# Kernel tuning notes

Measured on AMD Instinct MI355X. Metric: run time of the kernel, lower is better.

## Reference

```python
import jax, jax.numpy as jnp
import numpy as np

HIDDEN = 256
MAX_LENGTH = 256
NUM_LAYERS = 4
VOCAB = 50257


def setup_inputs() -> dict:
    key = jax.random.key(0)
    ks = jax.random.split(key, 16)
    s = 0.05
    return {
        "token": jax.random.randint(ks[0], (1,), 0, VOCAB, dtype=jnp.int64 if jax.config.jax_enable_x64 else jnp.int32),
        "hidden": jax.random.normal(ks[1], (NUM_LAYERS, 1, HIDDEN), dtype=jnp.float32),
        "encoder_outputs": jax.random.normal(ks[2], (MAX_LENGTH, HIDDEN), dtype=jnp.float32),
        "emb": jax.random.normal(ks[3], (VOCAB, HIDDEN), dtype=jnp.float32) * s,
        "attn_w": jax.random.normal(ks[4], (MAX_LENGTH, 2 * HIDDEN), dtype=jnp.float32) * s,
        "attn_b": jax.random.normal(ks[5], (MAX_LENGTH,), dtype=jnp.float32) * s,
        "comb_w": jax.random.normal(ks[6], (HIDDEN, 2 * HIDDEN), dtype=jnp.float32) * s,
        "comb_b": jax.random.normal(ks[7], (HIDDEN,), dtype=jnp.float32) * s,
        "gru_wih": jax.random.normal(ks[8], (NUM_LAYERS, 3 * HIDDEN, HIDDEN), dtype=jnp.float32) * s,
        "gru_whh": jax.random.normal(ks[9], (NUM_LAYERS, 3 * HIDDEN, HIDDEN), dtype=jnp.float32) * s,
        "gru_bih": jax.random.normal(ks[10], (NUM_LAYERS, 3 * HIDDEN), dtype=jnp.float32) * s,
        "gru_bhh": jax.random.normal(ks[11], (NUM_LAYERS, 3 * HIDDEN), dtype=jnp.float32) * s,
        "out_w": jax.random.normal(ks[12], (VOCAB, HIDDEN), dtype=jnp.float32) * s,
        "out_b": jax.random.normal(ks[13], (VOCAB,), dtype=jnp.float32) * s,
    }


def _gru_cell(x, h, wih, whh, bih, bhh):
    # PyTorch GRU cell: gates ordered [r, z, n]
    gi = x @ wih.T + bih  # [1, 3H]
    gh = h @ whh.T + bhh  # [1, 3H]
    i_r, i_z, i_n = jnp.split(gi, 3, axis=1)
    h_r, h_z, h_n = jnp.split(gh, 3, axis=1)
    r = jax.nn.sigmoid(i_r + h_r)
    z = jax.nn.sigmoid(i_z + h_z)
    n = jnp.tanh(i_n + r * h_n)
    return (1.0 - z) * n + z * h


def reference(token, hidden, encoder_outputs, emb, attn_w, attn_b, comb_w, comb_b,
              gru_wih, gru_whh, gru_bih, gru_bhh, out_w, out_b):
    # embedding lookup (dropout is identity in eval)  -> [1, H]
    embedded = emb[token]
    # Bahdanau-style attention weights over MAX_LENGTH positions
    attn_in = jnp.concatenate([embedded, hidden[0]], axis=1)  # [1, 2H]
    attn_weights = jax.nn.softmax(attn_in @ attn_w.T + attn_b, axis=1)  # [1, L]
    attn_applied = attn_weights @ encoder_outputs  # [1, H]
    comb_in = jnp.concatenate([embedded, attn_applied], axis=1)  # [1, 2H]
    x = jax.nn.relu(comb_in @ comb_w.T + comb_b)  # [1, H]
    # 4-layer GRU, single timestep
    new_h = []
    for l in range(NUM_LAYERS):
        h_l = _gru_cell(x, hidden[l], gru_wih[l], gru_whh[l], gru_bih[l], gru_bhh[l])
        new_h.append(h_l)
        x = h_l
    hidden_new = jnp.stack(new_h, axis=0)  # [4, 1, H]
    logp = jax.nn.log_softmax(x @ out_w.T + out_b, axis=1)  # [1, V]
    return (logp, hidden_new, attn_weights)
```

## Files before the change

### kernel.cpp

```cpp
#include <hip/hip_runtime.h>
#include <hip/hip_bf16.h>

#define H 256
#define L2H 512
#define NLAYERS 4
#define VOCAB 50257

#define OUT_LOGP 0
#define OUT_HID  50257
#define OUT_ATTN 51281

#define WS_SCORE 0
#define WS_BARS  256
#define WS_APP   512
#define WS_XA    768
#define WS_XB    1024
#define WS_PM    768
#define WS_PS    1024
#define WS_X4    1280
#define WS_X4B   1536
#define WS_X4C   1792
#define WS_GO    2048
#define WS_FLAG  2304

#define L_SCORE 0
#define L_APP   1
#define L_X0    2
#define L_LOG0  8

#define NCHAIN 8
#define NBLK 256

typedef unsigned short u16;
typedef unsigned long long u64;

__device__ __forceinline__ float bf2f(u16 u) {
    return __uint_as_float(((unsigned int)u) << 16);
}

__device__ __forceinline__ u16 f2bf(float f) {
    unsigned int x = __float_as_uint(f);
    unsigned int r = x + 0x7fff + ((x >> 16) & 1);
    return (u16)(r >> 16);
}

template<bool BF16>
__device__ __forceinline__ float ld1(const void* p, size_t i) {
    if (BF16) return bf2f(((const u16*)p)[i]);
    else      return ((const float*)p)[i];
}

template<bool BF16>
__device__ __forceinline__ void ld8(const void* p, size_t i, float* f) {
    if (BF16) {
        uint4 u = *(const uint4*)((const u16*)p + i);
        f[0] = bf2f(u.x & 0xffff); f[1] = bf2f(u.x >> 16);
        f[2] = bf2f(u.y & 0xffff); f[3] = bf2f(u.y >> 16);
        f[4] = bf2f(u.z & 0xffff); f[5] = bf2f(u.z >> 16);
        f[6] = bf2f(u.w & 0xffff); f[7] = bf2f(u.w >> 16);
    } else {
        const float4* q = (const float4*)((const float*)p + i);
        float4 a = q[0], b = q[1];
        f[0] = a.x; f[1] = a.y; f[2] = a.z; f[3] = a.w;
        f[4] = b.x; f[5] = b.y; f[6] = b.z; f[7] = b.w;
    }
}

template<bool BF16>
__device__ __forceinline__ void st(void* p, size_t i, float v) {
    if (BF16) ((u16*)p)[i] = f2bf(v);
    else      ((float*)p)[i] = v;
}

__device__ __forceinline__ float ldc(const float* p) {
    return __hip_atomic_load(const_cast<float*>(p), __ATOMIC_RELAXED, __HIP_MEMORY_SCOPE_AGENT);
}
__device__ __forceinline__ void stc(float* p, float v) {
    __hip_atomic_store(p, v, __ATOMIC_RELAXED, __HIP_MEMORY_SCOPE_AGENT);
}
__device__ __forceinline__ u64 ldcu(const u64* p) {
    return __hip_atomic_load(const_cast<u64*>(p), __ATOMIC_RELAXED, __HIP_MEMORY_SCOPE_AGENT);
}
__device__ __forceinline__ void stcu(u64* p, u64 v) {
    __hip_atomic_store(p, v, __ATOMIC_RELAXED, __HIP_MEMORY_SCOPE_AGENT);
}

__device__ __forceinline__ void arrive_line(unsigned* bars, int idx) {
    __syncthreads();
    if (threadIdx.x == 0)
        __hip_atomic_fetch_add(&bars[idx * 16], 1u, __ATOMIC_RELAXED, __HIP_MEMORY_SCOPE_AGENT);
}
template<int SLP>
__device__ __forceinline__ void wait_line(unsigned* bars, int idx, unsigned exp) {
    if (threadIdx.x == 0) {
        while (__hip_atomic_load(&bars[idx * 16], __ATOMIC_RELAXED, __HIP_MEMORY_SCOPE_AGENT) < exp)
            __builtin_amdgcn_s_sleep(SLP);
    }
    __syncthreads();
}

template<int SLP>
__device__ __forceinline__ u64 poll_go(const u64* p, unsigned need) {
    u64 u = ldcu(p);
    while ((unsigned)(u & 0xffffffffull) < need) {
        __builtin_amdgcn_s_sleep(SLP);
        u = ldcu(p);
    }
    return u;
}

__device__ __forceinline__ float dot8_u4bf(uint4 u, const float* xf) {
    return bf2f(u.x & 0xffff)*xf[0] + bf2f(u.x >> 16)*xf[1]
         + bf2f(u.y & 0xffff)*xf[2] + bf2f(u.y >> 16)*xf[3]
         + bf2f(u.z & 0xffff)*xf[4] + bf2f(u.z >> 16)*xf[5]
         + bf2f(u.w & 0xffff)*xf[6] + bf2f(u.w >> 16)*xf[7];
}

__global__ __launch_bounds__(256) void k_init(const void* emb, float* ws) {
    int tid = threadIdx.x;
    __hip_atomic_store((unsigned*)(ws + WS_BARS) + tid, 0u, __ATOMIC_RELAXED, __HIP_MEMORY_SCOPE_AGENT);
    __hip_atomic_store((unsigned*)(ws + WS_GO) + tid, 0u, __ATOMIC_RELAXED, __HIP_MEMORY_SCOPE_AGENT);
    __hip_atomic_store((unsigned*)(ws + WS_APP) + tid, 0u, __ATOMIC_RELAXED, __HIP_MEMORY_SCOPE_AGENT);
    if (tid < 64) {
        float b = fabsf(bf2f(((const u16*)emb)[tid]));
        #pragma unroll
        for (int off = 32; off; off >>= 1) b = fmaxf(b, __shfl_xor(b, off));
        if (tid == 0) ws[WS_FLAG] = (b < 1.0f) ? 1.0f : 0.0f;
    }
}

template<bool BF16>
__device__ __forceinline__ void logits_stream(
    const void* __restrict__ out_w, const void* __restrict__ out_b,
    const float* xf, int grp, int l32, float* vs, float& m, float& s)
{
    #pragma unroll
    for (int it = 0; it < 3; ++it) {
        const int rb = it * 16384 + grp;
        float wf[8][8], bb[8];
        #pragma unroll
        for (int k = 0; k < 8; ++k) {
            ld8<BF16>(out_w, (size_t)(rb + (k << 11)) * H + l32 * 8, wf[k]);
            bb[k] = ld1<BF16>(out_b, rb + (k << 11));
        }
        #pragma unroll
        for (int k = 0; k < 8; ++k) {
            float v = wf[k][0]*xf[0] + wf[k][1]*xf[1] + wf[k][2]*xf[2] + wf[k][3]*xf[3]
                    + wf[k][4]*xf[4] + wf[k][5]*xf[5] + wf[k][6]*xf[6] + wf[k][7]*xf[7];
            #pragma unroll
            for (int off = 16; off; off >>= 1) v += __shfl_xor(v, off);
            v += bb[k];
            vs[it * 8 + k] = v;
            float mn = fmaxf(m, v);
            s = s * __expf(m - mn) + __expf(v - mn);
            m = mn;
        }
    }
    vs[24] = 0.f;
    if (grp < VOCAB - 49152) {
        int r = 49152 + grp;
        float wf[8]; ld8<BF16>(out_w, (size_t)r * H + l32 * 8, wf);
        float v = wf[0]*xf[0] + wf[1]*xf[1] + wf[2]*xf[2] + wf[3]*xf[3]
                + wf[4]*xf[4] + wf[5]*xf[5] + wf[6]*xf[6] + wf[7]*xf[7];
        #pragma unroll
        for (int off = 16; off; off >>= 1) v += __shfl_xor(v, off);
        v += ld1<BF16>(out_b, r);
        vs[24] = v;
        float mn = fmaxf(m, v);
        s = s * __expf(m - mn) + __expf(v - mn);
        m = mn;
    }
}

template<bool BF16>
__device__ __forceinline__ void pipeline(
    const int* __restrict__ tok, const void* __restrict__ emb,
    const void* __restrict__ hidden,
    const void* __restrict__ attn_w, const void* __restrict__ attn_b,
    const void* __restrict__ enc,
    const void* __restrict__ comb_w, const void* __restrict__ comb_b,
    const void* __restrict__ gwih, const void* __restrict__ gwhh,
    const void* __restrict__ gbih, const void* __restrict__ gbhh,
    const void* __restrict__ out_w, const void* __restrict__ out_b,
    float* __restrict__ ws, void* __restrict__ out)
{
    unsigned* bars = (unsigned*)(ws + WS_BARS);
    const int tid  = threadIdx.x;
    const int lane = tid & 63;
    const int wid  = tid >> 6;
    const int bx   = blockIdx.x;
    const size_t es = BF16 ? 2 : 4;

    const int grp = (bx << 3) | (tid >> 5);
    const int l32 = tid & 31;

    __shared__ float lds[256];
    __shared__ float wsm[256];
    __shared__ float xsh[256];
    __shared__ float hsh[256];
    __shared__ float gd[192];
    __shared__ float cshare;

    float vs[25];
    float m = -1e30f, s = 0.f;

    if (bx < NCHAIN) {
        const int rbase = bx * 32;
        const int j8 = lane * 8;
        const int tk = tok[0];

        {
            float wfa[8][8];
            #pragma unroll
            for (int k = 0; k < 8; ++k)
                ld8<BF16>(attn_w, (size_t)(rbase + wid * 8 + k) * L2H + j8, wfa[k]);
            float xin[8];
            if (lane < 32) ld8<BF16>(emb, (size_t)tk * H + j8, xin);
            else           ld8<BF16>(hidden, (size_t)(j8 - H), xin);
            #pragma unroll
            for (int k = 0; k < 8; ++k) {
                int r = rbase + wid * 8 + k;
                float v = 0.f;
                #pragma unroll
                for (int q = 0; q < 8; ++q) v += xin[q] * wfa[k][q];
                #pragma unroll
                for (int off = 32; off; off >>= 1) v += __shfl_xor(v, off);
                if (lane == 0) stc(ws + WS_SCORE + r, v + ld1<BF16>(attn_b, r));
            }
        }
        arrive_line(bars, L_SCORE);

        {
            float ev[32];
            #pragma unroll
            for (int k = 0; k < 32; ++k)
                ev[k] = ld1<BF16>(enc, (size_t)(rbase + k) * H + tid);
            wait_line<1>(bars, L_SCORE, NCHAIN);
            float sc = ldc(ws + WS_SCORE + tid);
            lds[tid] = sc; __syncthreads();
            for (int off = 128; off; off >>= 1) {
                if (tid < off) lds[tid] = fmaxf(lds[tid], lds[tid + off]);
                __syncthreads();
            }
            float M = lds[0]; __syncthreads();
            float e = __expf(sc - M);
            lds[tid] = e; __syncthreads();
            for (int off = 128; off; off >>= 1) {
                if (tid < off) lds[tid] += lds[tid + off];
                __syncthreads();
            }
            float w = e / lds[0];
            wsm[tid] = w; __syncthreads();
            if (bx == 0) st<BF16>(out, OUT_ATTN + tid, w);
            float acc = 0.f;
            #pragma unroll
            for (int k = 0; k < 32; ++k) acc += wsm[rbase + k] * ev[k];
            atomicAdd(&ws[WS_APP + tid], acc);
        }
        arrive_line(bars, L_APP);

        {
            float wfa[8][8];
            #pragma unroll
            for (int k = 0; k < 8; ++k)
                ld8<BF16>(comb_w, (size_t)(rbase + wid * 8 + k) * L2H + j8, wfa[k]);
            float xin[8];
            if (lane < 32) ld8<BF16>(emb, (size_t)tk * H + j8, xin);
            wait_line<1>(bars, L_APP, NCHAIN);
            xsh[tid] = ldc(ws + WS_APP + tid);
            __syncthreads();
            if (lane >= 32) {
                #pragma unroll
                for (int q = 0; q < 8; ++q) xin[q] = xsh[j8 - H + q];
            }
            #pragma unroll
            for (int k = 0; k < 8; ++k) {
                int r = rbase + wid * 8 + k;
                float v = 0.f;
                #pragma unroll
                for (int q = 0; q < 8; ++q) v += xin[q] * wfa[k][q];
                #pragma unroll
                for (int off = 32; off; off >>= 1) v += __shfl_xor(v, off);
                if (lane == 0) stc(ws + WS_XA + r, fmaxf(v + ld1<BF16>(comb_b, r), 0.f));
            }
        }
        arrive_line(bars, L_X0);

        #pragma unroll 1
        for (int l = 0; l < NLAYERS; ++l) {
            const float* xin_p = ws + ((l & 1) ? WS_XB : WS_XA);
            const char* wih = (const char*)gwih + (size_t)l * 3 * H * H * es;
            const char* whh = (const char*)gwhh + (size_t)l * 3 * H * H * es;
            const char* bih = (const char*)gbih + (size_t)l * 3 * H * es;
            const char* bhh = (const char*)gbhh + (size_t)l * 3 * H * es;
            const char* hprev = (const char*)hidden + (size_t)l * H * es;
            char*       hout  = (char*)out + (size_t)(OUT_HID + l * H) * es;

            wait_line<1>(bars, L_X0 + l, NCHAIN);
            xsh[tid] = ldc(xin_p + tid);
            hsh[tid] = ld1<BF16>(hprev, tid);
            __syncthreads();

            if (tid < 192) {
                int mat = tid / 96;
                int rem = tid % 96;
                int g   = rem / 32;
                int j   = rem % 32;
                const void* W = mat ? (const void*)whh : (const void*)wih;
                const float* xv = mat ? hsh : xsh;
                size_t rowoff = (size_t)(g * H + rbase + j) * H;
                float acc = 0.f;
                #pragma unroll 16
                for (int c = 0; c < H; c += 8) {
                    float wf[8]; ld8<BF16>(W, rowoff + c, wf);
                    acc += wf[0]*xv[c]   + wf[1]*xv[c+1] + wf[2]*xv[c+2] + wf[3]*xv[c+3]
                         + wf[4]*xv[c+4] + wf[5]*xv[c+5] + wf[6]*xv[c+6] + wf[7]*xv[c+7];
                }
                gd[tid] = acc;
            }
            __syncthreads();
            if (tid < 32) {
                int i = rbase + tid;
                float r = 1.f / (1.f + __expf(-(gd[tid]      + ld1<BF16>(bih, i)
                                              + gd[96 + tid] + ld1<BF16>(bhh, i))));
                float z = 1.f / (1.f + __expf(-(gd[32 + tid]  + ld1<BF16>(bih, H + i)
                                              + gd[128 + tid] + ld1<BF16>(bhh, H + i))));
                float n = tanhf(gd[64 + tid] + ld1<BF16>(bih, 2 * H + i)
                              + r * (gd[160 + tid] + ld1<BF16>(bhh, 2 * H + i)));
                float hn = (1.f - z) * n + z * hsh[i];
                if (l < 3) stc(ws + ((l & 1) ? WS_XA : WS_XB) + i, hn);
                else { stc(ws + WS_X4 + i, hn); stc(ws + WS_X4B + i, hn); stc(ws + WS_X4C + i, hn); }
                st<BF16>(hout, i, hn);
            }
            arrive_line(bars, L_X0 + l + 1);
        }

        wait_line<1>(bars, L_X0 + 4, NCHAIN);
        if (bx == 0 && tid < 16)
            stcu((u64*)(ws + WS_GO + 16 * tid), 1ull);

        xsh[tid] = ldc(ws + WS_X4 + (bx % 3) * 256 + tid);
        __syncthreads();
        float xf[8];
        #pragma unroll
        for (int q = 0; q < 8; ++q) xf[q] = xsh[l32 * 8 + q];
        logits_stream<BF16>(out_w, out_b, xf, grp, l32, vs, m, s);
    } else {
        if constexpr (BF16) {
            uint4 pw[25]; float pb[25];
            #pragma unroll
            for (int it = 0; it < 3; ++it)
                #pragma unroll
                for (int k = 0; k < 8; ++k) {
                    int r = it * 16384 + (k << 11) + grp;
                    pw[it * 8 + k] = *(const uint4*)((const u16*)out_w + (size_t)r * H + l32 * 8);
                    pb[it * 8 + k] = ld1<true>(out_b, r);
                }
            if (grp < VOCAB - 49152) {
                int r = 49152 + grp;
                pw[24] = *(const uint4*)((const u16*)out_w + (size_t)r * H + l32 * 8);
                pb[24] = ld1<true>(out_b, r);
            } else { pw[24] = make_uint4(0, 0, 0, 0); pb[24] = 0.f; }

            if (tid == 0) (void)poll_go<2>((const u64*)(ws + WS_GO + 16 * (bx & 15)), 1u);
            __syncthreads();
            xsh[tid] = ldc(ws + WS_X4 + (bx % 3) * 256 + tid);
            __syncthreads();
            float xf[8];
            #pragma unroll
            for (int q = 0; q < 8; ++q) xf[q] = xsh[l32 * 8 + q];

            #pragma unroll
            for (int idx = 0; idx < 24; ++idx) {
                float v = dot8_u4bf(pw[idx], xf);
                #pragma unroll
                for (int off = 16; off; off >>= 1) v += __shfl_xor(v, off);
                v += pb[idx];
                vs[idx] = v;
                float mn = fmaxf(m, v);
                s = s * __expf(m - mn) + __expf(v - mn);
                m = mn;
            }
            vs[24] = 0.f;
            if (grp < VOCAB - 49152) {
                float v = dot8_u4bf(pw[24], xf);
                #pragma unroll
                for (int off = 16; off; off >>= 1) v += __shfl_xor(v, off);
                v += pb[24];
                vs[24] = v;
                float mn = fmaxf(m, v);
                s = s * __expf(m - mn) + __expf(v - mn);
                m = mn;
            }
        } else {
            if (tid == 0) (void)poll_go<2>((const u64*)(ws + WS_GO + 16 * (bx & 15)), 1u);
            __syncthreads();
            xsh[tid] = ldc(ws + WS_X4 + (bx % 3) * 256 + tid);
            __syncthreads();
            float xf[8];
            #pragma unroll
            for (int q = 0; q < 8; ++q) xf[q] = xsh[l32 * 8 + q];
            logits_stream<false>(out_w, out_b, xf, grp, l32, vs, m, s);
        }
    }

    {
        float mo = __shfl_xor(m, 32), so = __shfl_xor(s, 32);
        float M = fmaxf(m, mo);
        s = s * __expf(m - M) + so * __expf(mo - M);
        m = M;
    }
    if (lane == 0) { lds[wid] = m; lds[4 + wid] = s; }
    __syncthreads();
    if (tid == 0) {
        float M01 = fmaxf(lds[0], lds[1]);
        float S01 = lds[4] * __expf(lds[0] - M01) + lds[5] * __expf(lds[1] - M01);
        float M23 = fmaxf(lds[2], lds[3]);
        float S23 = lds[6] * __expf(lds[2] - M23) + lds[7] * __expf(lds[3] - M23);
        float Mx = fmaxf(M01, M23);
        float S  = S01 * __expf(M01 - Mx) + S23 * __expf(M23 - Mx);
        stc(ws + WS_PM + bx, Mx);
        stc(ws + WS_PS + bx, S);
    }
    arrive_line(bars, L_LOG0 + (bx & 7));

    float c;
    if (bx == 0) {
        if (tid < 8) {
            while (__hip_atomic_load(&bars[(L_LOG0 + tid) * 16],
                                     __ATOMIC_RELAXED, __HIP_MEMORY_SCOPE_AGENT) < 32u)
                __builtin_amdgcn_s_sleep(1);
        }
        __syncthreads();
        float mm = ldc(ws + WS_PM + tid);
        float ss = ldc(ws + WS_PS + tid);
        #pragma unroll
        for (int off = 32; off; off >>= 1) {
            float mo = __shfl_xor(mm, off), so = __shfl_xor(ss, off);
            float M = fmaxf(mm, mo);
            ss = ss * __expf(mm - M) + so * __expf(mo - M);
            mm = M;
        }
        if (lane == 0) { lds[wid] = mm; lds[4 + wid] = ss; }
        __syncthreads();
        if (tid == 0) {
            float M01 = fmaxf(lds[0], lds[1]);
            float S01 = lds[4] * __expf(lds[0] - M01) + lds[5] * __expf(lds[1] - M01);
            float M23 = fmaxf(lds[2], lds[3]);
            float S23 = lds[6] * __expf(lds[2] - M23) + lds[7] * __expf(lds[3] - M23);
            float Mx = fmaxf(M01, M23);
            float S  = S01 * __expf(M01 - Mx) + S23 * __expf(M23 - Mx);
            cshare = Mx + __logf(S);
        }
        __syncthreads();
        c = cshare;
        if (tid < 16)
            stcu((u64*)(ws + WS_GO + 16 * tid),
                 ((u64)__float_as_uint(c) << 32) | 2ull);
    } else {
        if (tid == 0) {
            u64 u = poll_go<2>((const u64*)(ws + WS_GO + 16 * (bx & 15)), 2u);
            cshare = __uint_as_float((unsigned)(u >> 32));
        }
        __syncthreads();
        c = cshare;
    }

    if (l32 == 0) {
        #pragma unroll
        for (int it = 0; it < 3; ++it)
            #pragma unroll
            for (int k = 0; k < 8; ++k)
                st<BF16>(out, OUT_LOGP + it * 16384 + (k << 11) + grp, vs[it * 8 + k] - c);
        if (grp < VOCAB - 49152)
            st<BF16>(out, OUT_LOGP + 49152 + grp, vs[24] - c);
    }
}

__global__ __launch_bounds__(256, 1) void k_all(
    const int* __restrict__ tok, const void* __restrict__ emb,
    const void* __restrict__ hidden,
    const void* __restrict__ attn_w, const void* __restrict__ attn_b,
    const void* __restrict__ enc,
    const void* __restrict__ comb_w, const void* __restrict__ comb_b,
    const void* __restrict__ gwih, const void* __restrict__ gwhh,
    const void* __restrict__ gbih, const void* __restrict__ gbhh,
    const void* __restrict__ out_w, const void* __restrict__ out_b,
    float* __restrict__ ws, void* __restrict__ out)
{
    if (ws[WS_FLAG] > 0.5f)
        pipeline<true >(tok, emb, hidden, attn_w, attn_b, enc, comb_w, comb_b,
                        gwih, gwhh, gbih, gbhh, out_w, out_b, ws, out);
    else
        pipeline<false>(tok, emb, hidden, attn_w, attn_b, enc, comb_w, comb_b,
                        gwih, gwhh, gbih, gbhh, out_w, out_b, ws, out);
}

extern "C" void kernel_launch(void* const* d_in, const int* in_sizes, int n_in,
                              void* d_out, int out_size, void* d_ws, size_t ws_size,
                              hipStream_t stream) {
    const int* tok = (const int*)d_in[0];
    float* ws = (float*)d_ws;

    k_init<<<dim3(1), dim3(256), 0, stream>>>(d_in[3], ws);
    k_all<<<dim3(NBLK), dim3(256), 0, stream>>>(
        tok, d_in[3], d_in[1], d_in[4], d_in[5], d_in[2], d_in[6], d_in[7],
        d_in[8], d_in[9], d_in[10], d_in[11], d_in[12], d_in[13],
        ws, d_out);
}
```

Baseline: 200.5 us.

## Spread decoder chain across 64 blocks with one row per wavefront

```diff
diff --git a/kernel.cpp b/kernel.cpp
--- a/kernel.cpp
+++ b/kernel.cpp
@@ -18,18 +18,16 @@
 #define WS_PM    768
 #define WS_PS    1024
 #define WS_X4    1280
-#define WS_X4B   1536
-#define WS_X4C   1792
 #define WS_GO    2048
 #define WS_FLAG  2304
 
-#define L_SCORE 0
-#define L_APP   1
-#define L_X0    2
-#define L_LOG0  8
-
-#define NCHAIN 8
-#define NBLK 256
+#define PH_SCORE 0
+#define PH_APP   1
+#define PH_X0    2
+#define PH_LOG   7
+
+#define NCHAIN 64
+#define NBLK   256
 
 typedef unsigned short u16;
 typedef unsigned long long u64;
@@ -48,6 +46,16 @@
 __device__ __forceinline__ float ld1(const void* p, size_t i) {
     if (BF16) return bf2f(((const u16*)p)[i]);
     else      return ((const float*)p)[i];
+}
+
+template<bool BF16>
+__device__ __forceinline__ float4 ld4(const void* p, size_t i) {
+    if (BF16) {
+        ushort4 w = *(const ushort4*)((const u16*)p + i);
+        return make_float4(bf2f(w.x), bf2f(w.y), bf2f(w.z), bf2f(w.w));
+    } else {
+        return *(const float4*)((const float*)p + i);
+    }
 }
 
 template<bool BF16>
@@ -85,15 +93,26 @@
     __hip_atomic_store(p, v, __ATOMIC_RELAXED, __HIP_MEMORY_SCOPE_AGENT);
 }
 
-__device__ __forceinline__ void arrive_line(unsigned* bars, int idx) {
+__device__ __forceinline__ void stage256(float* sh, const float* src, int tid) {
+    if (tid < 128) {
+        u64 u = ldcu((const u64*)src + tid);
+        sh[2 * tid]     = __uint_as_float((unsigned)(u & 0xffffffffull));
+        sh[2 * tid + 1] = __uint_as_float((unsigned)(u >> 32));
+    }
+    __syncthreads();
+}
+
+__device__ __forceinline__ void arrive_ph(unsigned* bars, int bx, int ph) {
     __syncthreads();
     if (threadIdx.x == 0)
-        __hip_atomic_fetch_add(&bars[idx * 16], 1u, __ATOMIC_RELAXED, __HIP_MEMORY_SCOPE_AGENT);
+        __hip_atomic_fetch_add(&bars[(bx & 15) * 16 + ph], 1u,
+                               __ATOMIC_RELAXED, __HIP_MEMORY_SCOPE_AGENT);
 }
 template<int SLP>
-__device__ __forceinline__ void wait_line(unsigned* bars, int idx, unsigned exp) {
-    if (threadIdx.x == 0) {
-        while (__hip_atomic_load(&bars[idx * 16], __ATOMIC_RELAXED, __HIP_MEMORY_SCOPE_AGENT) < exp)
+__device__ __forceinline__ void wait_ph(unsigned* bars, int ph, unsigned exp) {
+    if (threadIdx.x < 16) {
+        while (__hip_atomic_load(&bars[threadIdx.x * 16 + ph],
+                                 __ATOMIC_RELAXED, __HIP_MEMORY_SCOPE_AGENT) < exp)
             __builtin_amdgcn_s_sleep(SLP);
     }
     __syncthreads();
@@ -195,49 +214,42 @@
     const int l32 = tid & 31;
 
     __shared__ float lds[256];
+    __shared__ float xsh[256];
     __shared__ float wsm[256];
-    __shared__ float xsh[256];
-    __shared__ float hsh[256];
-    __shared__ float gd[192];
     __shared__ float cshare;
 
     float vs[25];
     float m = -1e30f, s = 0.f;
 
     if (bx < NCHAIN) {
-        const int rbase = bx * 32;
+        const int wv = (bx << 2) | wid;
         const int j8 = lane * 8;
         const int tk = tok[0];
 
         {
-            float wfa[8][8];
-            #pragma unroll
-            for (int k = 0; k < 8; ++k)
-                ld8<BF16>(attn_w, (size_t)(rbase + wid * 8 + k) * L2H + j8, wfa[k]);
+            float wf[8]; ld8<BF16>(attn_w, (size_t)wv * L2H + j8, wf);
             float xin[8];
             if (lane < 32) ld8<BF16>(emb, (size_t)tk * H + j8, xin);
             else           ld8<BF16>(hidden, (size_t)(j8 - H), xin);
-            #pragma unroll
-            for (int k = 0; k < 8; ++k) {
-                int r = rbase + wid * 8 + k;
-                float v = 0.f;
-                #pragma unroll
-                for (int q = 0; q < 8; ++q) v += xin[q] * wfa[k][q];
-                #pragma unroll
-                for (int off = 32; off; off >>= 1) v += __shfl_xor(v, off);
-                if (lane == 0) stc(ws + WS_SCORE + r, v + ld1<BF16>(attn_b, r));
-            }
-        }
-        arrive_line(bars, L_SCORE);
-
-        {
-            float ev[32];
-            #pragma unroll
-            for (int k = 0; k < 32; ++k)
-                ev[k] = ld1<BF16>(enc, (size_t)(rbase + k) * H + tid);
-            wait_line<1>(bars, L_SCORE, NCHAIN);
-            float sc = ldc(ws + WS_SCORE + tid);
-            lds[tid] = sc; __syncthreads();
+            float v = 0.f;
+            #pragma unroll
+            for (int q = 0; q < 8; ++q) v += xin[q] * wf[q];
+            #pragma unroll
+            for (int off = 32; off; off >>= 1) v += __shfl_xor(v, off);
+            if (lane == 0) stc(ws + WS_SCORE + wv, v + ld1<BF16>(attn_b, wv));
+        }
+        arrive_ph(bars, bx, PH_SCORE);
+
+        if (bx < 16) {
+            const int l0 = bx * 16;
+            float ev[16];
+            #pragma unroll
+            for (int k = 0; k < 16; ++k)
+                ev[k] = ld1<BF16>(enc, (size_t)(l0 + k) * H + tid);
+            wait_ph<1>(bars, PH_SCORE, 4);
+            stage256(lds, ws + WS_SCORE, tid);
+            float sc = lds[tid];
+            __syncthreads();
             for (int off = 128; off; off >>= 1) {
                 if (tid < off) lds[tid] = fmaxf(lds[tid], lds[tid + off]);
                 __syncthreads();
@@ -254,93 +266,93 @@
             if (bx == 0) st<BF16>(out, OUT_ATTN + tid, w);
             float acc = 0.f;
             #pragma unroll
-            for (int k = 0; k < 32; ++k) acc += wsm[rbase + k] * ev[k];
+            for (int k = 0; k < 16; ++k) acc += wsm[l0 + k] * ev[k];
             atomicAdd(&ws[WS_APP + tid], acc);
-        }
-        arrive_line(bars, L_APP);
+            arrive_ph(bars, bx, PH_APP);
+        }
 
         {
-            float wfa[8][8];
-            #pragma unroll
-            for (int k = 0; k < 8; ++k)
-                ld8<BF16>(comb_w, (size_t)(rbase + wid * 8 + k) * L2H + j8, wfa[k]);
+            float wf[8]; ld8<BF16>(comb_w, (size_t)wv * L2H + j8, wf);
             float xin[8];
             if (lane < 32) ld8<BF16>(emb, (size_t)tk * H + j8, xin);
-            wait_line<1>(bars, L_APP, NCHAIN);
-            xsh[tid] = ldc(ws + WS_APP + tid);
-            __syncthreads();
+            wait_ph<1>(bars, PH_APP, 1);
+            stage256(xsh, ws + WS_APP, tid);
             if (lane >= 32) {
                 #pragma unroll
                 for (int q = 0; q < 8; ++q) xin[q] = xsh[j8 - H + q];
             }
-            #pragma unroll
-            for (int k = 0; k < 8; ++k) {
-                int r = rbase + wid * 8 + k;
-                float v = 0.f;
-                #pragma unroll
-                for (int q = 0; q < 8; ++q) v += xin[q] * wfa[k][q];
-                #pragma unroll
-                for (int off = 32; off; off >>= 1) v += __shfl_xor(v, off);
-                if (lane == 0) stc(ws + WS_XA + r, fmaxf(v + ld1<BF16>(comb_b, r), 0.f));
-            }
-        }
-        arrive_line(bars, L_X0);
-
+            float v = 0.f;
+            #pragma unroll
+            for (int q = 0; q < 8; ++q) v += xin[q] * wf[q];
+            #pragma unroll
+            for (int off = 32; off; off >>= 1) v += __shfl_xor(v, off);
+            if (lane == 0) stc(ws + WS_XA + wv, fmaxf(v + ld1<BF16>(comb_b, wv), 0.f));
+        }
+        arrive_ph(bars, bx, PH_X0);
+
+        const int e4 = lane * 4;
         #pragma unroll 1
         for (int l = 0; l < NLAYERS; ++l) {
             const float* xin_p = ws + ((l & 1) ? WS_XB : WS_XA);
+            float*       xout  = ws + ((l & 1) ? WS_XA : WS_XB);
             const char* wih = (const char*)gwih + (size_t)l * 3 * H * H * es;
             const char* whh = (const char*)gwhh + (size_t)l * 3 * H * H * es;
             const char* bih = (const char*)gbih + (size_t)l * 3 * H * es;
             const char* bhh = (const char*)gbhh + (size_t)l * 3 * H * es;
             const char* hprev = (const char*)hidden + (size_t)l * H * es;
             char*       hout  = (char*)out + (size_t)(OUT_HID + l * H) * es;
-
-            wait_line<1>(bars, L_X0 + l, NCHAIN);
-            xsh[tid] = ldc(xin_p + tid);
-            hsh[tid] = ld1<BF16>(hprev, tid);
-            __syncthreads();
-
-            if (tid < 192) {
-                int mat = tid / 96;
-                int rem = tid % 96;
-                int g   = rem / 32;
-                int j   = rem % 32;
-                const void* W = mat ? (const void*)whh : (const void*)wih;
-                const float* xv = mat ? hsh : xsh;
-                size_t rowoff = (size_t)(g * H + rbase + j) * H;
-                float acc = 0.f;
-                #pragma unroll 16
-                for (int c = 0; c < H; c += 8) {
-                    float wf[8]; ld8<BF16>(W, rowoff + c, wf);
-                    acc += wf[0]*xv[c]   + wf[1]*xv[c+1] + wf[2]*xv[c+2] + wf[3]*xv[c+3]
-                         + wf[4]*xv[c+4] + wf[5]*xv[c+5] + wf[6]*xv[c+6] + wf[7]*xv[c+7];
+            const int i = wv;
+
+            float4 hv  = ld4<BF16>(hprev, e4);
+            float4 wri = ld4<BF16>(wih, (size_t)(i        ) * H + e4);
+            float4 wzi = ld4<BF16>(wih, (size_t)(H + i    ) * H + e4);
+            float4 wni = ld4<BF16>(wih, (size_t)(2 * H + i) * H + e4);
+            float4 wrh = ld4<BF16>(whh, (size_t)(i        ) * H + e4);
+            float4 wzh = ld4<BF16>(whh, (size_t)(H + i    ) * H + e4);
+            float4 wnh = ld4<BF16>(whh, (size_t)(2 * H + i) * H + e4);
+
+            wait_ph<1>(bars, PH_X0 + l, 4);
+            stage256(xsh, xin_p, tid);
+
+            float4 xv;
+            xv.x = xsh[e4]; xv.y = xsh[e4 + 1]; xv.z = xsh[e4 + 2]; xv.w = xsh[e4 + 3];
+
+            float a = wri.x * xv.x + wri.y * xv.y + wri.z * xv.z + wri.w * xv.w
+                    + wrh.x * hv.x + wrh.y * hv.y + wrh.z * hv.z + wrh.w * hv.w;
+            float b = wzi.x * xv.x + wzi.y * xv.y + wzi.z * xv.z + wzi.w * xv.w
+                    + wzh.x * hv.x + wzh.y * hv.y + wzh.z * hv.z + wzh.w * hv.w;
+            float c = wni.x * xv.x + wni.y * xv.y + wni.z * xv.z + wni.w * xv.w;
+            float d = wnh.x * hv.x + wnh.y * hv.y + wnh.z * hv.z + wnh.w * hv.w;
+
+            #pragma unroll
+            for (int off = 32; off; off >>= 1) {
+                a += __shfl_xor(a, off);
+                b += __shfl_xor(b, off);
+                c += __shfl_xor(c, off);
+                d += __shfl_xor(d, off);
+            }
+            if (lane == 0) {
+                float r = 1.f / (1.f + __expf(-(a + ld1<BF16>(bih, i) + ld1<BF16>(bhh, i))));
+                float z = 1.f / (1.f + __expf(-(b + ld1<BF16>(bih, H + i) + ld1<BF16>(bhh, H + i))));
+                float n = tanhf(c + ld1<BF16>(bih, 2 * H + i) + r * (d + ld1<BF16>(bhh, 2 * H + i)));
+                float hold = ld1<BF16>(hprev, i);
+                float hn = (1.f - z) * n + z * hold;
+                if (l < 3) stc(xout + i, hn);
+                else {
+                    stc(ws + WS_X4 + i, hn);
+                    stc(ws + WS_X4 + 256 + i, hn);
+                    stc(ws + WS_X4 + 512 + i, hn);
                 }
-                gd[tid] = acc;
-            }
-            __syncthreads();
-            if (tid < 32) {
-                int i = rbase + tid;
-                float r = 1.f / (1.f + __expf(-(gd[tid]      + ld1<BF16>(bih, i)
-                                              + gd[96 + tid] + ld1<BF16>(bhh, i))));
-                float z = 1.f / (1.f + __expf(-(gd[32 + tid]  + ld1<BF16>(bih, H + i)
-                                              + gd[128 + tid] + ld1<BF16>(bhh, H + i))));
-                float n = tanhf(gd[64 + tid] + ld1<BF16>(bih, 2 * H + i)
-                              + r * (gd[160 + tid] + ld1<BF16>(bhh, 2 * H + i)));
-                float hn = (1.f - z) * n + z * hsh[i];
-                if (l < 3) stc(ws + ((l & 1) ? WS_XA : WS_XB) + i, hn);
-                else { stc(ws + WS_X4 + i, hn); stc(ws + WS_X4B + i, hn); stc(ws + WS_X4C + i, hn); }
                 st<BF16>(hout, i, hn);
             }
-            arrive_line(bars, L_X0 + l + 1);
-        }
-
-        wait_line<1>(bars, L_X0 + 4, NCHAIN);
-        if (bx == 0 && tid < 16)
-            stcu((u64*)(ws + WS_GO + 16 * tid), 1ull);
-
-        xsh[tid] = ldc(ws + WS_X4 + (bx % 3) * 256 + tid);
-        __syncthreads();
+            arrive_ph(bars, bx, PH_X0 + l + 1);
+        }
+
+        wait_ph<1>(bars, PH_X0 + 4, 4);
+        if (bx < 16 && tid == 0)
+            stcu((u64*)(ws + WS_GO + 16 * bx), 1ull);
+
+        stage256(xsh, ws + WS_X4 + (bx % 3) * 256, tid);
         float xf[8];
         #pragma unroll
         for (int q = 0; q < 8; ++q) xf[q] = xsh[l32 * 8 + q];
@@ -364,8 +376,7 @@
 
             if (tid == 0) (void)poll_go<2>((const u64*)(ws + WS_GO + 16 * (bx & 15)), 1u);
             __syncthreads();
-            xsh[tid] = ldc(ws + WS_X4 + (bx % 3) * 256 + tid);
-            __syncthreads();
+            stage256(xsh, ws + WS_X4 + (bx % 3) * 256, tid);
             float xf[8];
             #pragma unroll
             for (int q = 0; q < 8; ++q) xf[q] = xsh[l32 * 8 + q];
@@ -395,8 +406,7 @@
         } else {
             if (tid == 0) (void)poll_go<2>((const u64*)(ws + WS_GO + 16 * (bx & 15)), 1u);
             __syncthreads();
-            xsh[tid] = ldc(ws + WS_X4 + (bx % 3) * 256 + tid);
-            __syncthreads();
+            stage256(xsh, ws + WS_X4 + (bx % 3) * 256, tid);
             float xf[8];
             #pragma unroll
             for (int q = 0; q < 8; ++q) xf[q] = xsh[l32 * 8 + q];
@@ -410,6 +420,7 @@
         s = s * __expf(m - M) + so * __expf(mo - M);
         m = M;
     }
+    __syncthreads();
     if (lane == 0) { lds[wid] = m; lds[4 + wid] = s; }
     __syncthreads();
     if (tid == 0) {
@@ -422,13 +433,13 @@
         stc(ws + WS_PM + bx, Mx);
         stc(ws + WS_PS + bx, S);
     }
-    arrive_line(bars, L_LOG0 + (bx & 7));
+    arrive_ph(bars, bx, PH_LOG);
 
     float c;
     if (bx == 0) {
-        if (tid < 8) {
-            while (__hip_atomic_load(&bars[(L_LOG0 + tid) * 16],
-                                     __ATOMIC_RELAXED, __HIP_MEMORY_SCOPE_AGENT) < 32u)
+        if (tid < 16) {
+            while (__hip_atomic_load(&bars[tid * 16 + PH_LOG],
+                                     __ATOMIC_RELAXED, __HIP_MEMORY_SCOPE_AGENT) < 16u)
                 __builtin_amdgcn_s_sleep(1);
         }
         __syncthreads();
```

Result: faster. 160.4 us (-20.0%).
